# Kernel tuning notes

Hardware: AMD Instinct MI355X
Metric: run time of the kernel (lower is better)

Reference implementation:

```python
import jax, jax.numpy as jnp
import numpy as np

S, C, H, D = 4096, 2048, 16, 128  # seq, channels, heads, head_dim
EPS = 1.1920929e-07  # torch F.rms_norm default eps = finfo(float32).eps


def setup_inputs() -> dict:
    key = jax.random.key(0)
    ks = jax.random.split(key, 12)
    w = 0.02
    return {
        "x": jax.random.normal(ks[0], (S, C), dtype=jnp.float32),
        "rope": jax.random.normal(ks[1], (S, 1, D // 2, 2, 2), dtype=jnp.float32),
        "Wq": jax.random.normal(ks[2], (C, C), dtype=jnp.float32) * w,
        "bq": jnp.zeros((C,), dtype=jnp.float32),
        "Wk": jax.random.normal(ks[3], (C, C), dtype=jnp.float32) * w,
        "bk": jnp.zeros((C,), dtype=jnp.float32),
        "Wv": jax.random.normal(ks[4], (C, C), dtype=jnp.float32) * w,
        "bv": jnp.zeros((C,), dtype=jnp.float32),
        "qn_w": jnp.ones((D,), dtype=jnp.float32),
        "kn_w": jnp.ones((D,), dtype=jnp.float32),
        "Wo": jax.random.normal(ks[5], (C, C), dtype=jnp.float32) * w,
        "bo": jnp.zeros((C,), dtype=jnp.float32),
    }


def _rms_norm(x, weight):
    # RMSNorm over last dim, as F.rms_norm
    inv = jax.lax.rsqrt(jnp.mean(x * x, axis=-1, keepdims=True) + EPS)
    return x * inv * weight


def _apply_rotary(x, rope):
    # x: [S, H, D]; rope: [S, 1, D//2, 2, 2]
    s, h, d = x.shape
    x_ = x.reshape(s, h, d // 2, 1, 2)
    out = (rope * x_).sum(axis=-1)  # [S, H, D//2, 2]
    return out.reshape(s, h, d)


def reference(x, rope, Wq, bq, Wk, bk, Wv, bv, qn_w, kn_w, Wo, bo):
    # QKV projections -> [S, H, D]
    q = (x @ Wq.T + bq).reshape(S, H, D)
    k = (x @ Wk.T + bk).reshape(S, H, D)
    v = (x @ Wv.T + bv).reshape(S, H, D)
    # RMSNorm on q/k per head_dim
    q = _rms_norm(q, qn_w)
    k = _rms_norm(k, kn_w)
    # Custom rotary (table-driven 2x2 rotation)
    q = _apply_rotary(q, rope)
    k = _apply_rotary(k, rope)
    # Dense scaled dot-product attention over seq, per head
    scale = 1.0 / jnp.sqrt(jnp.asarray(D, dtype=q.dtype))
    scores = jnp.einsum("shd,thd->hst", q, k) * scale  # [H, S, S]
    probs = jax.nn.softmax(scores, axis=-1)
    out = jnp.einsum("hst,thd->shd", probs, v).reshape(S, C)
    return out @ Wo.T + bo
```

## Files before the change

kernel.cpp:

```cpp
#include <hip/hip_runtime.h>

#define S 4096
#define C 2048
#define H 16
#define D 128
#define EPS 1.1920929e-07f
#define QSCALE (0.08838834764831845f * 1.4426950408889634f)
#define BN 64
#define NT (S / BN)
#define GBM 256
#define GBN 128
#define GBK 64
#define NKT (C / GBK)
#define GBUF (GBM * GBK + GBN * GBK)

typedef __attribute__((ext_vector_type(8))) short short8;
typedef __attribute__((ext_vector_type(4))) float f32x4;
typedef __attribute__((ext_vector_type(4))) unsigned int uint4v;

#if __has_builtin(__builtin_amdgcn_exp2f)
#define EXP2F __builtin_amdgcn_exp2f
#else
#define EXP2F exp2f
#endif

__device__ __forceinline__ unsigned short f2bf(float f) {
  unsigned int u = __builtin_bit_cast(unsigned int, f);
  u += 0x7fff + ((u >> 16) & 1);
  return (unsigned short)(u >> 16);
}
__device__ __forceinline__ float bf2f(unsigned short v) {
  unsigned int u = ((unsigned int)v) << 16;
  return __builtin_bit_cast(float, u);
}
__device__ __forceinline__ unsigned int pkbf(float a, float b) {
  return (unsigned int)f2bf(a) | ((unsigned int)f2bf(b) << 16);
}
__device__ __forceinline__ unsigned int pkbf_trunc(float a, float b) {
  return __builtin_amdgcn_perm(__builtin_bit_cast(unsigned int, b),
                               __builtin_bit_cast(unsigned int, a), 0x07060302);
}
__device__ __forceinline__ void gld16(const unsigned short* g, unsigned short* l) {
  __builtin_amdgcn_global_load_lds(
      (const __attribute__((address_space(1))) unsigned int*)g,
      (__attribute__((address_space(3))) unsigned int*)l, 16, 0, 0);
}
__device__ __forceinline__ short8 mk_a(unsigned int a, unsigned int b,
                                       unsigned int c, unsigned int d) {
  uint4v u;
  u[0] = a; u[1] = b; u[2] = c; u[3] = d;
  return __builtin_bit_cast(short8, u);
}

__global__ void cvt_kernel(const float* __restrict__ src,
                           unsigned short* __restrict__ dst, int n) {
  int i = (blockIdx.x * 256 + threadIdx.x) * 4;
  if (i >= n) return;
  float4 v = *(const float4*)(src + i);
  ushort4 o;
  o.x = f2bf(v.x); o.y = f2bf(v.y); o.z = f2bf(v.z); o.w = f2bf(v.w);
  *(ushort4*)(dst + i) = o;
}
__global__ void cvtw_kernel(const float* __restrict__ w0, const float* __restrict__ w1,
                            const float* __restrict__ w2, const float* __restrict__ w3,
                            unsigned short* __restrict__ dst) {
  const float* srcs[4] = {w0, w1, w2, w3};
  const float* src = srcs[blockIdx.y];
  int i = (blockIdx.x * 256 + threadIdx.x) * 4;
  float4 v = *(const float4*)(src + i);
  ushort4 o;
  o.x = f2bf(v.x); o.y = f2bf(v.y); o.z = f2bf(v.z); o.w = f2bf(v.w);
  *(ushort4*)(dst + (size_t)blockIdx.y * C * C + i) = o;
}
__global__ void bias_concat(const float* __restrict__ bq, const float* __restrict__ bk,
                            const float* __restrict__ bv, float* __restrict__ dst) {
  int i = blockIdx.x * 256 + threadIdx.x;
  const float* s = (i < C) ? bq : ((i < 2 * C) ? bk : bv);
  dst[i] = s[i & (C - 1)];
}

__global__ __launch_bounds__(512, 2) void gemm_bt(const unsigned short* __restrict__ A,
                                                  const unsigned short* __restrict__ B,
                                                  const float* __restrict__ bias,
                                                  float* __restrict__ outf,
                                                  unsigned short* __restrict__ qh,
                                                  unsigned short* __restrict__ kh,
                                                  unsigned short* __restrict__ vt,
                                                  int N, int mode) {
  __shared__ __align__(16) unsigned short L[3 * GBUF];
  const int t = threadIdx.x, w = t >> 6, lane = t & 63;
  const int lq = lane & 15, quad = lane >> 4;
  const int wm = w >> 1, wn = w & 1;

  const int nwg = gridDim.x * gridDim.y;
  int id = blockIdx.x * gridDim.y + blockIdx.y;
  int nid = (id & 7) * (nwg >> 3) + (id >> 3);
  const int bx = nid / (int)gridDim.y, by = nid % (int)gridDim.y;
  const int m0 = by * GBM, n0 = bx * GBN;

  f32x4 acc[4][4] = {};
  float biasv[4];
#pragma unroll
  for (int nt = 0; nt < 4; nt++) biasv[nt] = bias[n0 + wn * 64 + nt * 16 + lq];

  const int srow = lane >> 3, sg = lane & 7;
  auto stage = [&](int tt, int b) {
    unsigned short* Ab = L + b * GBUF;
    unsigned short* Bb = Ab + GBM * GBK;
    const int k0 = tt * GBK;
#pragma unroll
    for (int p = 0; p < 4; p++) {
      int row = p * 64 + w * 8 + srow;
      int c = sg ^ (row & 7);
      gld16(A + (size_t)(m0 + row) * C + k0 + c * 8, Ab + (p * 64 + w * 8) * GBK);
    }
#pragma unroll
    for (int p = 0; p < 2; p++) {
      int row = p * 64 + w * 8 + srow;
      int c = sg ^ (row & 7);
      gld16(B + (size_t)(n0 + row) * C + k0 + c * 8, Bb + (p * 64 + w * 8) * GBK);
    }
  };

  stage(0, 0);
  stage(1, 1);

  int cb = 0;
  for (int tt = 0; tt < NKT; ++tt) {
    if (tt < NKT - 1)
      asm volatile("s_waitcnt vmcnt(6)" ::: "memory");
    else
      asm volatile("s_waitcnt vmcnt(0)" ::: "memory");
    __builtin_amdgcn_s_barrier();
    asm volatile("" ::: "memory");
    if (tt + 2 < NKT) {
      int sb = cb + 2; if (sb >= 3) sb -= 3;
      stage(tt + 2, sb);
    }
    unsigned short* Ab = L + cb * GBUF;
    unsigned short* Bb = Ab + GBM * GBK;
    short8 af[4][2], bf[4][2];
#pragma unroll
    for (int mt = 0; mt < 4; mt++) {
      int row = wm * 64 + mt * 16 + lq;
#pragma unroll
      for (int ks = 0; ks < 2; ks++)
        af[mt][ks] = *(const short8*)&Ab[row * GBK + (((ks * 4 + quad) ^ (row & 7)) * 8)];
    }
#pragma unroll
    for (int nt = 0; nt < 4; nt++) {
      int row = wn * 64 + nt * 16 + lq;
#pragma unroll
      for (int ks = 0; ks < 2; ks++)
        bf[nt][ks] = *(const short8*)&Bb[row * GBK + (((ks * 4 + quad) ^ (row & 7)) * 8)];
    }
    __builtin_amdgcn_s_setprio(1);
#pragma unroll
    for (int ks = 0; ks < 2; ks++)
#pragma unroll
      for (int mt = 0; mt < 4; mt++)
#pragma unroll
        for (int nt = 0; nt < 4; nt++)
          acc[mt][nt] = __builtin_amdgcn_mfma_f32_16x16x32_bf16(af[mt][ks], bf[nt][ks], acc[mt][nt], 0, 0, 0);
    __builtin_amdgcn_s_setprio(0);
    cb = (cb == 2) ? 0 : cb + 1;
  }

  if (mode == 0) {
#pragma unroll
    for (int mt = 0; mt < 4; mt++)
#pragma unroll
      for (int nt = 0; nt < 4; nt++) {
        int n = n0 + wn * 64 + nt * 16 + lq;
#pragma unroll
        for (int r = 0; r < 4; r++) {
          int m = m0 + wm * 64 + mt * 16 + quad * 4 + r;
          outf[(size_t)m * N + n] = acc[mt][nt][r] + biasv[nt];
        }
      }
    return;
  }

  const int gh = bx;
  __syncthreads();
  if (gh < 32) {
    unsigned short* U = L;
#pragma unroll
    for (int mt = 0; mt < 4; mt++)
#pragma unroll
      for (int nt = 0; nt < 4; nt++) {
        int dloc = wn * 64 + nt * 16 + lq;
#pragma unroll
        for (int r = 0; r < 4; r++)
          U[(wm * 64 + mt * 16 + quad * 4 + r) * 136 + dloc] = f2bf(acc[mt][nt][r] + biasv[nt]);
      }
    __syncthreads();
    unsigned short* dst = ((gh < 16) ? qh : kh) + (size_t)(gh & 15) * S * D;
    const int rr = t >> 4, ck = t & 15;
#pragma unroll
    for (int p = 0; p < 8; p++) {
      int m = p * 32 + rr;
      uint4 vv = *(const uint4*)&U[m * 136 + ck * 8];
      *(uint4*)(dst + (size_t)(m0 + m) * D + ck * 8) = vv;
    }
  } else {
    unsigned short* U = L;
#pragma unroll
    for (int mt = 0; mt < 4; mt++)
#pragma unroll
      for (int nt = 0; nt < 4; nt++) {
        int dloc = wn * 64 + nt * 16 + lq;
        int mlocP = wm * 64 + (mt >> 1) * 32 + quad * 8 + (mt & 1) * 4;
        *(unsigned int*)&U[dloc * 264 + mlocP] =
            pkbf(acc[mt][nt][0] + biasv[nt], acc[mt][nt][1] + biasv[nt]);
        *(unsigned int*)&U[dloc * 264 + mlocP + 2] =
            pkbf(acc[mt][nt][2] + biasv[nt], acc[mt][nt][3] + biasv[nt]);
      }
    __syncthreads();
    unsigned short* dst = vt + (size_t)(gh - 32) * D * S;
    const int rr = t >> 5, ck = t & 31;
#pragma unroll
    for (int p = 0; p < 8; p++) {
      int d = p * 16 + rr;
      uint4 vv = *(const uint4*)&U[d * 264 + ck * 8];
      *(uint4*)(dst + (size_t)d * S + m0 + ck * 8) = vv;
    }
  }
}

__global__ __launch_bounds__(256) void rmsrope_kernel(unsigned short* __restrict__ qh,
                                                      unsigned short* __restrict__ kh,
                                                      const float* __restrict__ qn_w,
                                                      const float* __restrict__ kn_w,
                                                      const float* __restrict__ rope) {
  const int which = blockIdx.y;
  unsigned short* io = which ? kh : qh;
  const float* wgt = which ? kn_w : qn_w;
  const float scale = which ? 1.0f : QSCALE;
  int wid = (blockIdx.x * 256 + threadIdx.x) >> 6;
  int lane = threadIdx.x & 63;
  int s = wid & (S - 1);
  unsigned short* row = io + (size_t)wid * D;
  unsigned int pr = *(unsigned int*)(row + lane * 2);
  float a = bf2f((unsigned short)(pr & 0xffff));
  float b = bf2f((unsigned short)(pr >> 16));
  float ss = a * a + b * b;
  for (int m = 1; m < 64; m <<= 1) ss += __shfl_xor(ss, m);
  float inv = rsqrtf(ss * (1.0f / 128.0f) + EPS) * scale;
  float2 wv = *(const float2*)(wgt + lane * 2);
  float an = a * inv * wv.x, bn = b * inv * wv.y;
  float4 r = *(const float4*)(rope + (size_t)s * 256 + lane * 4);
  *(unsigned int*)(row + lane * 2) = pkbf(r.x * an + r.y * bn, r.z * an + r.w * bn);
}

__global__ __launch_bounds__(256, 2) void flash_kernel(const unsigned short* __restrict__ qh,
                                                       const unsigned short* __restrict__ kh,
                                                       const unsigned short* __restrict__ vt,
                                                       unsigned short* __restrict__ ao) {
  __shared__ __align__(16) unsigned short Klds[2 * BN * D];
  __shared__ __align__(16) unsigned short Vlds[2 * D * BN];
  const int h = blockIdx.y, i0 = blockIdx.x * 128;
  const int t = threadIdx.x, w = t >> 6, lane = t & 63;
  const int lq = lane & 15, quad = lane >> 4;

  const unsigned short* Qbase = qh + ((size_t)h * S + i0 + w * 32 + lq) * D;
  short8 qfrag[2][4];
#pragma unroll
  for (int qi = 0; qi < 2; qi++)
#pragma unroll
    for (int kt = 0; kt < 4; kt++)
      qfrag[qi][kt] = *(const short8*)(Qbase + (size_t)qi * 16 * D + kt * 32 + quad * 8);

  f32x4 oacc[2][8] = {};
  f32x4 dacc[2] = {};
  const unsigned short* Kbase = kh + (size_t)h * S * D;
  const unsigned short* Vbase = vt + (size_t)h * D * S;

  const int k_r = lane >> 4, k_g = lane & 15;
  const int v_r = lane >> 3, v_g = lane & 7;

  uint4v onesu;
  onesu[0] = 0x3F803F80u; onesu[1] = 0x3F803F80u; onesu[2] = 0x3F803F80u; onesu[3] = 0x3F803F80u;
  const short8 ones = __builtin_bit_cast(short8, onesu);

#pragma unroll
  for (int p = 0; p < 4; p++) {
    int kr = w * 16 + p * 4 + k_r;
    gld16(Kbase + (size_t)kr * D + (k_g ^ (kr & 7)) * 8, &Klds[(w * 16 + p * 4) * D]);
  }
#pragma unroll
  for (int p = 0; p < 4; p++) {
    int vr = w * 32 + p * 8 + v_r;
    gld16(Vbase + (size_t)vr * S + (v_g ^ (vr & 7)) * 8, &Vlds[(w * 32 + p * 8) * BN]);
  }

  for (int tt = 0; tt < NT; ++tt) {
    const int cur = tt & 1;
    unsigned short* Kc = Klds + cur * (BN * D);
    unsigned short* Vc = Vlds + cur * (D * BN);
    __syncthreads();
    if (tt + 1 < NT) {
      const int j1 = (tt + 1) * BN;
      unsigned short* Kn = Klds + (cur ^ 1) * (BN * D);
      unsigned short* Vn = Vlds + (cur ^ 1) * (D * BN);
#pragma unroll
      for (int p = 0; p < 4; p++) {
        int kr = w * 16 + p * 4 + k_r;
        gld16(Kbase + (size_t)(j1 + kr) * D + (k_g ^ (kr & 7)) * 8, &Kn[(w * 16 + p * 4) * D]);
      }
#pragma unroll
      for (int p = 0; p < 4; p++) {
        int vr = w * 32 + p * 8 + v_r;
        gld16(Vbase + (size_t)vr * S + j1 + (v_g ^ (vr & 7)) * 8, &Vn[(w * 32 + p * 8) * BN]);
      }
    }

    f32x4 sacc[2][4] = {};
    __builtin_amdgcn_s_setprio(1);
#pragma unroll
    for (int kt = 0; kt < 4; kt++)
#pragma unroll
      for (int nt = 0; nt < 4; nt++) {
        int row = nt * 16 + lq;
        short8 af = *(const short8*)&Kc[row * D + (((kt * 4 + quad) ^ (row & 7)) * 8)];
        sacc[0][nt] = __builtin_amdgcn_mfma_f32_16x16x32_bf16(af, qfrag[0][kt], sacc[0][nt], 0, 0, 0);
        sacc[1][nt] = __builtin_amdgcn_mfma_f32_16x16x32_bf16(af, qfrag[1][kt], sacc[1][nt], 0, 0, 0);
      }
    __builtin_amdgcn_s_setprio(0);

    unsigned int pd[2][4][2];
#pragma unroll
    for (int qi = 0; qi < 2; qi++)
#pragma unroll
      for (int nt = 0; nt < 4; nt++) {
        float e0 = EXP2F(sacc[qi][nt][0]);
        float e1 = EXP2F(sacc[qi][nt][1]);
        float e2 = EXP2F(sacc[qi][nt][2]);
        float e3 = EXP2F(sacc[qi][nt][3]);
        pd[qi][nt][0] = pkbf_trunc(e0, e1);
        pd[qi][nt][1] = pkbf_trunc(e2, e3);
      }

    __builtin_amdgcn_s_setprio(1);
#pragma unroll
    for (int kk = 0; kk < 2; kk++) {
      short8 a0 = mk_a(pd[0][2 * kk][0], pd[0][2 * kk][1], pd[0][2 * kk + 1][0], pd[0][2 * kk + 1][1]);
      short8 a1 = mk_a(pd[1][2 * kk][0], pd[1][2 * kk][1], pd[1][2 * kk + 1][0], pd[1][2 * kk + 1][1]);
      dacc[0] = __builtin_amdgcn_mfma_f32_16x16x32_bf16(a0, ones, dacc[0], 0, 0, 0);
      dacc[1] = __builtin_amdgcn_mfma_f32_16x16x32_bf16(a1, ones, dacc[1], 0, 0, 0);
#pragma unroll
      for (int dt = 0; dt < 8; dt++) {
        int row = dt * 16 + lq;
        short8 bf = *(const short8*)&Vc[row * BN + (((kk * 4 + quad) ^ (row & 7)) * 8)];
        oacc[0][dt] = __builtin_amdgcn_mfma_f32_16x16x32_bf16(a0, bf, oacc[0][dt], 0, 0, 0);
        oacc[1][dt] = __builtin_amdgcn_mfma_f32_16x16x32_bf16(a1, bf, oacc[1][dt], 0, 0, 0);
      }
    }
    __builtin_amdgcn_s_setprio(0);
  }

  float il[2][4];
#pragma unroll
  for (int qi = 0; qi < 2; qi++)
#pragma unroll
    for (int r = 0; r < 4; r++) il[qi][r] = 1.0f / dacc[qi][r];
#pragma unroll
  for (int qi = 0; qi < 2; qi++)
#pragma unroll
    for (int dt = 0; dt < 8; dt++)
#pragma unroll
      for (int r = 0; r < 4; r++)
        ao[(size_t)(i0 + w * 32 + qi * 16 + quad * 4 + r) * C + h * 128 + dt * 16 + lq] =
            f2bf(oacc[qi][dt][r] * il[qi][r]);
}

extern "C" void kernel_launch(void* const* d_in, const int* in_sizes, int n_in,
                              void* d_out, int out_size, void* d_ws, size_t ws_size,
                              hipStream_t stream) {
  const float* x    = (const float*)d_in[0];
  const float* rope = (const float*)d_in[1];
  const float* Wq   = (const float*)d_in[2];
  const float* bq   = (const float*)d_in[3];
  const float* Wk   = (const float*)d_in[4];
  const float* bk   = (const float*)d_in[5];
  const float* Wv   = (const float*)d_in[6];
  const float* bv   = (const float*)d_in[7];
  const float* qn_w = (const float*)d_in[8];
  const float* kn_w = (const float*)d_in[9];
  const float* Wo   = (const float*)d_in[10];
  const float* bo   = (const float*)d_in[11];
  float* out = (float*)d_out;

  unsigned short* xb  = (unsigned short*)d_ws;
  unsigned short* wqb = xb + (size_t)S * C;
  unsigned short* wob = wqb + (size_t)3 * C * C;
  unsigned short* qh  = wqb + (size_t)4 * C * C;
  unsigned short* kh  = qh + (size_t)S * C;
  unsigned short* vt  = kh + (size_t)S * C;
  unsigned short* ao  = vt + (size_t)S * C;
  float* bqkv = (float*)(ao + (size_t)S * C);

  cvt_kernel<<<S * C / 1024, 256, 0, stream>>>(x, xb, S * C);
  cvtw_kernel<<<dim3(C * C / 1024, 4), 256, 0, stream>>>(Wq, Wk, Wv, Wo, wqb);
  bias_concat<<<3 * C / 256, 256, 0, stream>>>(bq, bk, bv, bqkv);

  gemm_bt<<<dim3(3 * C / GBN, S / GBM), 512, 0, stream>>>(
      xb, wqb, bqkv, nullptr, qh, kh, vt, 3 * C, 1);

  rmsrope_kernel<<<dim3((H * S) / 4, 2), 256, 0, stream>>>(qh, kh, qn_w, kn_w, rope);

  flash_kernel<<<dim3(S / 128, H), 256, 0, stream>>>(qh, kh, vt, ao);

  gemm_bt<<<dim3(C / GBN, S / GBM), 512, 0, stream>>>(
      ao, wob, bo, out, nullptr, nullptr, nullptr, C, 0);
}
```

Before: 439.9 us.

## Split flash attention key tile across wave pairs with LDS reduction of partials

Each wave now handles 64 query rows but only half of each 64-key tile, instead of 32 query rows over the full tile. Pairs of waves combine their partial output and denominator accumulators through shared memory at the end. The aim is to reuse each K and V fragment read from LDS across four query tiles instead of two, which cuts LDS read traffic per MFMA. In exchange, accumulator register pressure doubles (oacc goes to 4x8), which risks spills or lower occupancy under launch_bounds(256,2), and the epilogue gains extra LDS round trips and barriers.

```diff
diff --git a/kernel.cpp b/kernel.cpp
--- a/kernel.cpp
+++ b/kernel.cpp
@@ -257,22 +257,24 @@
                                                        const unsigned short* __restrict__ kh,
                                                        const unsigned short* __restrict__ vt,
                                                        unsigned short* __restrict__ ao) {
-  __shared__ __align__(16) unsigned short Klds[2 * BN * D];
-  __shared__ __align__(16) unsigned short Vlds[2 * D * BN];
+  __shared__ __align__(16) unsigned short LdsAll[2 * BN * D + 2 * D * BN];
+  unsigned short* Klds = LdsAll;
+  unsigned short* Vlds = LdsAll + 2 * BN * D;
   const int h = blockIdx.y, i0 = blockIdx.x * 128;
   const int t = threadIdx.x, w = t >> 6, lane = t & 63;
   const int lq = lane & 15, quad = lane >> 4;
-
-  const unsigned short* Qbase = qh + ((size_t)h * S + i0 + w * 32 + lq) * D;
-  short8 qfrag[2][4];
-#pragma unroll
-  for (int qi = 0; qi < 2; qi++)
+  const int wr = w >> 1, kkw = w & 1;
+
+  const unsigned short* Qbase = qh + ((size_t)h * S + i0 + wr * 64 + lq) * D;
+  short8 qfrag[4][4];
+#pragma unroll
+  for (int qi = 0; qi < 4; qi++)
 #pragma unroll
     for (int kt = 0; kt < 4; kt++)
       qfrag[qi][kt] = *(const short8*)(Qbase + (size_t)qi * 16 * D + kt * 32 + quad * 8);
 
-  f32x4 oacc[2][8] = {};
-  f32x4 dacc[2] = {};
+  f32x4 oacc[4][8] = {};
+  f32x4 dacc[4] = {};
   const unsigned short* Kbase = kh + (size_t)h * S * D;
   const unsigned short* Vbase = vt + (size_t)h * D * S;
 
@@ -315,63 +317,89 @@
       }
     }
 
-    f32x4 sacc[2][4] = {};
+    f32x4 sacc[4][2] = {};
     __builtin_amdgcn_s_setprio(1);
 #pragma unroll
     for (int kt = 0; kt < 4; kt++)
 #pragma unroll
-      for (int nt = 0; nt < 4; nt++) {
-        int row = nt * 16 + lq;
+      for (int ntl = 0; ntl < 2; ntl++) {
+        int row = (kkw * 2 + ntl) * 16 + lq;
         short8 af = *(const short8*)&Kc[row * D + (((kt * 4 + quad) ^ (row & 7)) * 8)];
-        sacc[0][nt] = __builtin_amdgcn_mfma_f32_16x16x32_bf16(af, qfrag[0][kt], sacc[0][nt], 0, 0, 0);
-        sacc[1][nt] = __builtin_amdgcn_mfma_f32_16x16x32_bf16(af, qfrag[1][kt], sacc[1][nt], 0, 0, 0);
+#pragma unroll
+        for (int qi = 0; qi < 4; qi++)
+          sacc[qi][ntl] = __builtin_amdgcn_mfma_f32_16x16x32_bf16(af, qfrag[qi][kt], sacc[qi][ntl], 0, 0, 0);
       }
     __builtin_amdgcn_s_setprio(0);
 
-    unsigned int pd[2][4][2];
-#pragma unroll
-    for (int qi = 0; qi < 2; qi++)
-#pragma unroll
-      for (int nt = 0; nt < 4; nt++) {
-        float e0 = EXP2F(sacc[qi][nt][0]);
-        float e1 = EXP2F(sacc[qi][nt][1]);
-        float e2 = EXP2F(sacc[qi][nt][2]);
-        float e3 = EXP2F(sacc[qi][nt][3]);
-        pd[qi][nt][0] = pkbf_trunc(e0, e1);
-        pd[qi][nt][1] = pkbf_trunc(e2, e3);
+    unsigned int pd[4][2][2];
+#pragma unroll
+    for (int qi = 0; qi < 4; qi++)
+#pragma unroll
+      for (int ntl = 0; ntl < 2; ntl++) {
+        float e0 = EXP2F(sacc[qi][ntl][0]);
+        float e1 = EXP2F(sacc[qi][ntl][1]);
+        float e2 = EXP2F(sacc[qi][ntl][2]);
+        float e3 = EXP2F(sacc[qi][ntl][3]);
+        pd[qi][ntl][0] = pkbf_trunc(e0, e1);
+        pd[qi][ntl][1] = pkbf_trunc(e2, e3);
       }
 
     __builtin_amdgcn_s_setprio(1);
-#pragma unroll
-    for (int kk = 0; kk < 2; kk++) {
-      short8 a0 = mk_a(pd[0][2 * kk][0], pd[0][2 * kk][1], pd[0][2 * kk + 1][0], pd[0][2 * kk + 1][1]);
-      short8 a1 = mk_a(pd[1][2 * kk][0], pd[1][2 * kk][1], pd[1][2 * kk + 1][0], pd[1][2 * kk + 1][1]);
-      dacc[0] = __builtin_amdgcn_mfma_f32_16x16x32_bf16(a0, ones, dacc[0], 0, 0, 0);
-      dacc[1] = __builtin_amdgcn_mfma_f32_16x16x32_bf16(a1, ones, dacc[1], 0, 0, 0);
+    {
+      short8 a[4];
+#pragma unroll
+      for (int qi = 0; qi < 4; qi++) {
+        a[qi] = mk_a(pd[qi][0][0], pd[qi][0][1], pd[qi][1][0], pd[qi][1][1]);
+        dacc[qi] = __builtin_amdgcn_mfma_f32_16x16x32_bf16(a[qi], ones, dacc[qi], 0, 0, 0);
+      }
 #pragma unroll
       for (int dt = 0; dt < 8; dt++) {
         int row = dt * 16 + lq;
-        short8 bf = *(const short8*)&Vc[row * BN + (((kk * 4 + quad) ^ (row & 7)) * 8)];
-        oacc[0][dt] = __builtin_amdgcn_mfma_f32_16x16x32_bf16(a0, bf, oacc[0][dt], 0, 0, 0);
-        oacc[1][dt] = __builtin_amdgcn_mfma_f32_16x16x32_bf16(a1, bf, oacc[1][dt], 0, 0, 0);
+        short8 bf = *(const short8*)&Vc[row * BN + (((kkw * 4 + quad) ^ (row & 7)) * 8)];
+#pragma unroll
+        for (int qi = 0; qi < 4; qi++)
+          oacc[qi][dt] = __builtin_amdgcn_mfma_f32_16x16x32_bf16(a[qi], bf, oacc[qi][dt], 0, 0, 0);
       }
     }
     __builtin_amdgcn_s_setprio(0);
   }
 
-  float il[2][4];
-#pragma unroll
-  for (int qi = 0; qi < 2; qi++)
-#pragma unroll
-    for (int r = 0; r < 4; r++) il[qi][r] = 1.0f / dacc[qi][r];
-#pragma unroll
-  for (int qi = 0; qi < 2; qi++)
-#pragma unroll
-    for (int dt = 0; dt < 8; dt++)
-#pragma unroll
-      for (int r = 0; r < 4; r++)
-        ao[(size_t)(i0 + w * 32 + qi * 16 + quad * 4 + r) * C + h * 128 + dt * 16 + lq] =
-            f2bf(oacc[qi][dt][r] * il[qi][r]);
+  __syncthreads();
+  float* Lf = (float*)LdsAll;
+#pragma unroll
+  for (int qp = 0; qp < 2; qp++) {
+    if (kkw) {
+#pragma unroll
+      for (int qj = 0; qj < 2; qj++) {
+        int qi = qp * 2 + qj;
+        float* dstl = Lf + (qj * 2 + wr) * (64 * 37) + lane * 37;
+#pragma unroll
+        for (int dt = 0; dt < 8; dt++)
+#pragma unroll
+          for (int r = 0; r < 4; r++) dstl[dt * 4 + r] = oacc[qi][dt][r];
+#pragma unroll
+        for (int r = 0; r < 4; r++) dstl[32 + r] = dacc[qi][r];
+      }
+    }
+    __syncthreads();
+    if (!kkw) {
+#pragma unroll
+      for (int qj = 0; qj < 2; qj++) {
+        int qi = qp * 2 + qj;
+        const float* srcl = Lf + (qj * 2 + wr) * (64 * 37) + lane * 37;
+        float il[4];
+#pragma unroll
+        for (int r = 0; r < 4; r++) il[r] = 1.0f / (dacc[qi][r] + srcl[32 + r]);
+#pragma unroll
+        for (int dt = 0; dt < 8; dt++)
+#pragma unroll
+          for (int r = 0; r < 4; r++)
+            ao[(size_t)(i0 + wr * 64 + qi * 16 + quad * 4 + r) * C + h * 128 + dt * 16 + lq] =
+                f2bf((oacc[qi][dt][r] + srcl[dt * 4 + r]) * il[r]);
+      }
+    }
+    __syncthreads();
+  }
 }
 
 extern "C" void kernel_launch(void* const* d_in, const int* in_sizes, int n_in,
```

Result: slower. 570.1 us (+29.6%).
